# Kernel optimization log

Measured on AMD Instinct MI355X. Metric: run time of the kernel, lower is better.

Reference implementation:

```python
import jax, jax.numpy as jnp
import numpy as np

N = 50000          # nodes
E = 1_600_000      # edges (avg degree 32)
D = 128            # in_channels
H = 4              # heads
C = 32             # out_channels per head (H*C == D for residual add)
NEG_SLOPE = 0.2
STEPS = 3


def setup_inputs() -> dict:
    key = jax.random.key(0)
    k1, k2, k3, k4, k5 = jax.random.split(key, 5)
    x = jax.random.normal(k1, (N, D), jnp.float32)
    edge_index = jax.random.randint(k2, (2, E), 0, N)  # row0=src, row1=dst
    W = jax.random.normal(k3, (D, H * C), jnp.float32) * (1.0 / np.sqrt(D))
    a_src = jax.random.normal(k4, (H, C), jnp.float32) * 0.1
    a_dst = jax.random.normal(k5, (H, C), jnp.float32) * 0.1
    return {"x": x, "edge_index": edge_index, "W": W,
            "a_src": a_src, "a_dst": a_dst, "steps": STEPS}


def _attn_conv(x, edge_index, W, a_src, a_dst):
    """One GAT-style attention conv. Returns (out [N,H*C], attn [E,H], logits [E,H])."""
    src, dst = edge_index[0], edge_index[1]
    h = (x @ W).reshape(N, H, C)                      # [N,H,C]
    alpha_src = jnp.einsum('nhc,hc->nh', h, a_src)    # [N,H]
    alpha_dst = jnp.einsum('nhc,hc->nh', h, a_dst)    # [N,H]
    logits = jax.nn.leaky_relu(alpha_src[src] + alpha_dst[dst], NEG_SLOPE)  # [E,H]
    # softmax over incoming edges of each destination node (segment softmax)
    m = jax.ops.segment_max(logits, dst, num_segments=N)      # [N,H]
    m = jnp.where(jnp.isfinite(m), m, 0.0)                    # nodes w/o in-edges
    e = jnp.exp(logits - m[dst])                              # [E,H]
    denom = jax.ops.segment_sum(e, dst, num_segments=N)       # [N,H]
    attn = e / (denom[dst] + 1e-16)                           # [E,H]
    msg = h[src] * attn[..., None]                            # [E,H,C]
    out = jax.ops.segment_sum(msg, dst, num_segments=N)       # [N,H,C]
    return out.reshape(N, H * C), attn, logits


def reference(x, edge_index, W, a_src, a_dst, steps):
    x_s, attn_s, rel_s = [], [], []
    for _ in range(steps):  # fixed small step count, matches the torch Python loop
        x_prime, attn_t, rel_t = _attn_conv(x, edge_index, W, a_src, a_dst)
        x = x + x_prime
        x_s.append(x)
        attn_s.append(attn_t)
        rel_s.append(rel_t)
    return jnp.stack(x_s, 0), jnp.stack(attn_s, 0), jnp.stack(rel_s, 0)
```

## Files before the change

### kernel.cpp

```cpp
#include <hip/hip_runtime.h>
#include <hip/hip_bf16.h>
#include <math.h>

#define NN 50000
#define EE 1600000
#define DD 128
#define HH 4
#define NSTEP 3
#define NEG 0.2f
#define BM 32
#define NPB 8
#define CAPN 96
#define MAXD 96

typedef unsigned short ushort8v __attribute__((ext_vector_type(8)));
typedef float float4v __attribute__((ext_vector_type(4)));

__device__ __forceinline__ float leaky(float v) { return v >= 0.0f ? v : NEG * v; }

__device__ __forceinline__ unsigned short bfu(float f) {
    __hip_bfloat16 b = __float2bfloat16(f);
    return *reinterpret_cast<unsigned short*>(&b);
}
__device__ __forceinline__ float ubf(unsigned short u) {
    return __uint_as_float(((unsigned int)u) << 16);
}

__global__ __launch_bounds__(256) void gemm_k2(const float* __restrict__ X,
                                               const float* __restrict__ W,
                                               const float* __restrict__ a_src,
                                               const float* __restrict__ a_dst,
                                               unsigned short* __restrict__ Hb,
                                               float* __restrict__ as_,
                                               float4* __restrict__ nd) {
    __shared__ float xs[BM][132];
    const int tid  = threadIdx.x;
    const int tcol = tid & 31;
    const int trow = tid >> 5;
    const int row0 = blockIdx.x * BM;

    #pragma unroll
    for (int i = 0; i < 4; ++i) {
        const int l  = tid + 256 * i;
        const int r  = l >> 5;
        const int c4 = l & 31;
        float4 v = {0.f, 0.f, 0.f, 0.f};
        if (row0 + r < NN) v = ((const float4*)(X + (size_t)(row0 + r) * DD))[c4];
        *(float4*)&xs[r][c4 * 4] = v;
    }
    __syncthreads();

    const float4* __restrict__ W4 = (const float4*)W;
    float4 acc0 = {0,0,0,0}, acc1 = {0,0,0,0}, acc2 = {0,0,0,0}, acc3 = {0,0,0,0};

    for (int k = 0; k < DD; k += 4) {
        float4 wv0 = W4[(k + 0) * 32 + tcol];
        float4 wv1 = W4[(k + 1) * 32 + tcol];
        float4 wv2 = W4[(k + 2) * 32 + tcol];
        float4 wv3 = W4[(k + 3) * 32 + tcol];
        float4 xv0 = *(const float4*)&xs[4 * trow + 0][k];
        float4 xv1 = *(const float4*)&xs[4 * trow + 1][k];
        float4 xv2 = *(const float4*)&xs[4 * trow + 2][k];
        float4 xv3 = *(const float4*)&xs[4 * trow + 3][k];
        #define GSTEP(ACC, XV) \
            ACC.x += XV.x * wv0.x; ACC.y += XV.x * wv0.y; ACC.z += XV.x * wv0.z; ACC.w += XV.x * wv0.w; \
            ACC.x += XV.y * wv1.x; ACC.y += XV.y * wv1.y; ACC.z += XV.y * wv1.z; ACC.w += XV.y * wv1.w; \
            ACC.x += XV.z * wv2.x; ACC.y += XV.z * wv2.y; ACC.z += XV.z * wv2.z; ACC.w += XV.z * wv2.w; \
            ACC.x += XV.w * wv3.x; ACC.y += XV.w * wv3.y; ACC.z += XV.w * wv3.z; ACC.w += XV.w * wv3.w;
        GSTEP(acc0, xv0) GSTEP(acc1, xv1) GSTEP(acc2, xv2) GSTEP(acc3, xv3)
        #undef GSTEP
    }

    const float4 asv = ((const float4*)a_src)[tcol];
    const float4 adv = ((const float4*)a_dst)[tcol];
    float ps0 = acc0.x*asv.x + acc0.y*asv.y + acc0.z*asv.z + acc0.w*asv.w;
    float ps1 = acc1.x*asv.x + acc1.y*asv.y + acc1.z*asv.z + acc1.w*asv.w;
    float ps2 = acc2.x*asv.x + acc2.y*asv.y + acc2.z*asv.z + acc2.w*asv.w;
    float ps3 = acc3.x*asv.x + acc3.y*asv.y + acc3.z*asv.z + acc3.w*asv.w;
    float pd0 = acc0.x*adv.x + acc0.y*adv.y + acc0.z*adv.z + acc0.w*adv.w;
    float pd1 = acc1.x*adv.x + acc1.y*adv.y + acc1.z*adv.z + acc1.w*adv.w;
    float pd2 = acc2.x*adv.x + acc2.y*adv.y + acc2.z*adv.z + acc2.w*adv.w;
    float pd3 = acc3.x*adv.x + acc3.y*adv.y + acc3.z*adv.z + acc3.w*adv.w;
    #pragma unroll
    for (int off = 1; off < 8; off <<= 1) {
        ps0 += __shfl_xor(ps0, off); ps1 += __shfl_xor(ps1, off);
        ps2 += __shfl_xor(ps2, off); ps3 += __shfl_xor(ps3, off);
        pd0 += __shfl_xor(pd0, off); pd1 += __shfl_xor(pd1, off);
        pd2 += __shfl_xor(pd2, off); pd3 += __shfl_xor(pd3, off);
    }

    #pragma unroll
    for (int i = 0; i < 4; ++i) {
        const int row = row0 + 4 * trow + i;
        if (row >= NN) break;
        const float4 a = (i == 0) ? acc0 : (i == 1) ? acc1 : (i == 2) ? acc2 : acc3;
        ushort4 p;
        p.x = bfu(a.x); p.y = bfu(a.y); p.z = bfu(a.z); p.w = bfu(a.w);
        *(ushort4*)&Hb[(size_t)row * DD + 4 * tcol] = p;
    }
    if ((tcol & 7) == 0) {
        const int head = tcol >> 3;
        #pragma unroll
        for (int i = 0; i < 4; ++i) {
            const int row = row0 + 4 * trow + i;
            if (row >= NN) break;
            const float ps = (i == 0) ? ps0 : (i == 1) ? ps1 : (i == 2) ? ps2 : ps3;
            const float pd = (i == 0) ? pd0 : (i == 1) ? pd1 : (i == 2) ? pd2 : pd3;
            as_[(size_t)row * HH + head] = ps;
            ((float*)(nd + (size_t)row * 3))[head] = pd;
        }
    }
}

__global__ __launch_bounds__(256) void zero_k(int* __restrict__ p, int n) {
    const int i = blockIdx.x * 256 + threadIdx.x;
    if (i < n) p[i] = 0;
}

__global__ __launch_bounds__(256) void scat_k(const int* __restrict__ ei,
                                              int* __restrict__ cursor,
                                              int* __restrict__ csr) {
    const int e = blockIdx.x * 256 + threadIdx.x;
    if (e >= EE) return;
    const int s = ei[e], d = ei[EE + e];
    const int pos = atomicAdd(&cursor[d], 1);
    if (pos < MAXD) csr[(size_t)d * MAXD + pos] = s;
}

__global__ __launch_bounds__(256) void node_k3(const int* __restrict__ cursor,
                                               const int* __restrict__ csr,
                                               const float* __restrict__ as_,
                                               float4* __restrict__ nd,
                                               const unsigned short* __restrict__ Hb,
                                               const float* __restrict__ xprev,
                                               float* __restrict__ xout) {
    __shared__ int    src_l[NPB][CAPN];
    __shared__ float4 exp_l[NPB][CAPN];

    const int tid  = threadIdx.x;
    const int nl   = tid >> 5;
    const int lane = tid & 31;
    const int n    = blockIdx.x * NPB + nl;

    int deg = cursor[n];
    if (deg > MAXD) deg = MAXD;
    const size_t row0 = (size_t)n * MAXD;

    if (deg == 0) {
        ((float4*)(xout + (size_t)n * DD))[lane] = ((const float4*)(xprev + (size_t)n * DD))[lane];
        return;
    }

    const float4 adv = nd[(size_t)n * 3];

    float4 mx = {-INFINITY, -INFINITY, -INFINITY, -INFINITY};
    for (int j = lane; j < deg; j += 32) {
        const int s = csr[row0 + j];
        const float4 av = *(const float4*)(as_ + (size_t)s * HH);
        float4 l;
        l.x = leaky(av.x + adv.x); l.y = leaky(av.y + adv.y);
        l.z = leaky(av.z + adv.z); l.w = leaky(av.w + adv.w);
        src_l[nl][j] = s; exp_l[nl][j] = l;
        mx.x = fmaxf(mx.x, l.x); mx.y = fmaxf(mx.y, l.y);
        mx.z = fmaxf(mx.z, l.z); mx.w = fmaxf(mx.w, l.w);
    }
    #pragma unroll
    for (int off = 1; off < 32; off <<= 1) {
        mx.x = fmaxf(mx.x, __shfl_xor(mx.x, off));
        mx.y = fmaxf(mx.y, __shfl_xor(mx.y, off));
        mx.z = fmaxf(mx.z, __shfl_xor(mx.z, off));
        mx.w = fmaxf(mx.w, __shfl_xor(mx.w, off));
    }

    float4 ds = {0.f, 0.f, 0.f, 0.f};
    for (int j = lane; j < deg; j += 32) {
        const float4 l = exp_l[nl][j];
        float4 e4;
        e4.x = expf(l.x - mx.x); e4.y = expf(l.y - mx.y);
        e4.z = expf(l.z - mx.z); e4.w = expf(l.w - mx.w);
        exp_l[nl][j] = e4;
        ds.x += e4.x; ds.y += e4.y; ds.z += e4.z; ds.w += e4.w;
    }
    #pragma unroll
    for (int off = 1; off < 32; off <<= 1) {
        ds.x += __shfl_xor(ds.x, off); ds.y += __shfl_xor(ds.y, off);
        ds.z += __shfl_xor(ds.z, off); ds.w += __shfl_xor(ds.w, off);
    }
    float4 inv;
    inv.x = 1.0f / (ds.x + 1e-16f); inv.y = 1.0f / (ds.y + 1e-16f);
    inv.z = 1.0f / (ds.z + 1e-16f); inv.w = 1.0f / (ds.w + 1e-16f);

    if (lane == 0) {
        nd[(size_t)n * 3 + 1] = mx;
        nd[(size_t)n * 3 + 2] = inv;
    }

    const int esel = lane >> 4;
    const int sub  = lane & 15;
    const int hsel = sub >> 2;
    const float invh = (hsel == 0) ? inv.x : (hsel == 1) ? inv.y : (hsel == 2) ? inv.z : inv.w;
    float4 aclo = {0.f, 0.f, 0.f, 0.f};
    float4 achi = {0.f, 0.f, 0.f, 0.f};
    int j0 = 0;
    #pragma unroll 2
    for (; j0 + 2 <= deg; j0 += 2) {
        const int j = j0 + esel;
        const int s = src_l[nl][j];
        const float a = ((const float*)&exp_l[nl][j])[hsel] * invh;
        const ushort8v hv = *(const ushort8v*)&Hb[(size_t)s * DD + 8 * sub];
        aclo.x += ubf(hv[0]) * a; aclo.y += ubf(hv[1]) * a;
        aclo.z += ubf(hv[2]) * a; aclo.w += ubf(hv[3]) * a;
        achi.x += ubf(hv[4]) * a; achi.y += ubf(hv[5]) * a;
        achi.z += ubf(hv[6]) * a; achi.w += ubf(hv[7]) * a;
    }
    if (j0 < deg && esel == 0) {
        const int j = j0;
        const int s = src_l[nl][j];
        const float a = ((const float*)&exp_l[nl][j])[hsel] * invh;
        const ushort8v hv = *(const ushort8v*)&Hb[(size_t)s * DD + 8 * sub];
        aclo.x += ubf(hv[0]) * a; aclo.y += ubf(hv[1]) * a;
        aclo.z += ubf(hv[2]) * a; aclo.w += ubf(hv[3]) * a;
        achi.x += ubf(hv[4]) * a; achi.y += ubf(hv[5]) * a;
        achi.z += ubf(hv[6]) * a; achi.w += ubf(hv[7]) * a;
    }
    aclo.x += __shfl_xor(aclo.x, 16); aclo.y += __shfl_xor(aclo.y, 16);
    aclo.z += __shfl_xor(aclo.z, 16); aclo.w += __shfl_xor(aclo.w, 16);
    achi.x += __shfl_xor(achi.x, 16); achi.y += __shfl_xor(achi.y, 16);
    achi.z += __shfl_xor(achi.z, 16); achi.w += __shfl_xor(achi.w, 16);
    const float4 mine = (esel == 0) ? aclo : achi;
    const int fidx = 2 * sub + esel;
    const float4 xv = ((const float4*)(xprev + (size_t)n * DD))[fidx];
    float4 o;
    o.x = xv.x + mine.x; o.y = xv.y + mine.y; o.z = xv.z + mine.z; o.w = xv.w + mine.w;
    ((float4*)(xout + (size_t)n * DD))[fidx] = o;
}

__global__ __launch_bounds__(256) void edgeattn3_k(const int* __restrict__ ei,
                                                   const float* __restrict__ as3,
                                                   const float4* __restrict__ nd3,
                                                   float* __restrict__ rel_out,
                                                   float* __restrict__ attn_out) {
    const int e = blockIdx.x * 256 + threadIdx.x;
    if (e >= EE) return;
    const int st = blockIdx.y;
    const int s = __builtin_nontemporal_load(ei + e);
    const int d = __builtin_nontemporal_load(ei + EE + e);
    const float4 av = *(const float4*)(as3 + ((size_t)st * NN + s) * HH);
    const float4* ndp = nd3 + ((size_t)st * NN + d) * 3;
    const float4 dv = ndp[0];
    const float4 mm = ndp[1];
    const float4 iv = ndp[2];
    float4v l;
    l.x = leaky(av.x + dv.x); l.y = leaky(av.y + dv.y);
    l.z = leaky(av.z + dv.z); l.w = leaky(av.w + dv.w);
    __builtin_nontemporal_store(l, (float4v*)(rel_out + ((size_t)st * EE + e) * HH));
    float4v a;
    a.x = expf(l.x - mm.x) * iv.x; a.y = expf(l.y - mm.y) * iv.y;
    a.z = expf(l.z - mm.z) * iv.z; a.w = expf(l.w - mm.w) * iv.w;
    __builtin_nontemporal_store(a, (float4v*)(attn_out + ((size_t)st * EE + e) * HH));
}

extern "C" void kernel_launch(void* const* d_in, const int* in_sizes, int n_in,
                              void* d_out, int out_size, void* d_ws, size_t ws_size,
                              hipStream_t stream) {
    const float* x     = (const float*)d_in[0];
    const int*   ei    = (const int*)d_in[1];
    const float* W     = (const float*)d_in[2];
    const float* a_src = (const float*)d_in[3];
    const float* a_dst = (const float*)d_in[4];

    float* xs_out   = (float*)d_out;
    float* attn_out = xs_out + (size_t)NSTEP * NN * DD;
    float* rel_out  = attn_out + (size_t)NSTEP * EE * HH;

    unsigned short* hb = (unsigned short*)d_ws;
    float*  as3   = (float*)(hb + (size_t)NN * DD);
    float4* nd3   = (float4*)(as3 + (size_t)NSTEP * NN * HH);
    int*    cursor = (int*)(nd3 + (size_t)NSTEP * NN * 3);
    int*    csr    = cursor + NN;

    zero_k<<<(NN + 255) / 256, 256, 0, stream>>>(cursor, NN);
    scat_k<<<(EE + 255) / 256, 256, 0, stream>>>(ei, cursor, csr);

    const float* xprev = x;
    for (int s = 0; s < NSTEP; ++s) {
        float* xs_s = xs_out + (size_t)s * NN * DD;
        float* as_  = as3 + (size_t)s * NN * HH;
        float4* nd  = nd3 + (size_t)s * NN * 3;

        gemm_k2<<<(NN + BM - 1) / BM, 256, 0, stream>>>(xprev, W, a_src, a_dst, hb, as_, nd);
        node_k3<<<NN / NPB, 256, 0, stream>>>(cursor, csr, as_, nd, hb, xprev, xs_s);
        xprev = xs_s;
    }
    dim3 eg((EE + 255) / 256, NSTEP);
    edgeattn3_k<<<eg, 256, 0, stream>>>(ei, as3, nd3, rel_out, attn_out);
}
```

Measured before the change: 502.3 us.

## Split per-node CSR into edge-hashed partitions with 16-bit source indices

```diff
diff --git a/kernel.cpp b/kernel.cpp
--- a/kernel.cpp
+++ b/kernel.cpp
@@ -10,8 +10,9 @@
 #define NEG 0.2f
 #define BM 32
 #define NPB 8
-#define CAPN 96
-#define MAXD 96
+#define CAPN 128
+#define NPART 4
+#define SEGC 32
 
 typedef unsigned short ushort8v __attribute__((ext_vector_type(8)));
 typedef float float4v __attribute__((ext_vector_type(4)));
@@ -119,16 +120,17 @@
 
 __global__ __launch_bounds__(256) void scat_k(const int* __restrict__ ei,
                                               int* __restrict__ cursor,
-                                              int* __restrict__ csr) {
+                                              unsigned short* __restrict__ csr) {
     const int e = blockIdx.x * 256 + threadIdx.x;
     if (e >= EE) return;
     const int s = ei[e], d = ei[EE + e];
-    const int pos = atomicAdd(&cursor[d], 1);
-    if (pos < MAXD) csr[(size_t)d * MAXD + pos] = s;
+    const int c = d * NPART + (e & (NPART - 1));
+    const int pos = atomicAdd(&cursor[c], 1);
+    if (pos < SEGC) csr[(size_t)c * SEGC + pos] = (unsigned short)s;
 }
 
 __global__ __launch_bounds__(256) void node_k3(const int* __restrict__ cursor,
-                                               const int* __restrict__ csr,
+                                               const unsigned short* __restrict__ csr,
                                                const float* __restrict__ as_,
                                                float4* __restrict__ nd,
                                                const unsigned short* __restrict__ Hb,
@@ -142,9 +144,16 @@
     const int lane = tid & 31;
     const int n    = blockIdx.x * NPB + nl;
 
-    int deg = cursor[n];
-    if (deg > MAXD) deg = MAXD;
-    const size_t row0 = (size_t)n * MAXD;
+    const int cbase = n * NPART;
+    int degs[NPART];
+    int deg = 0;
+    #pragma unroll
+    for (int p = 0; p < NPART; ++p) {
+        int dp = cursor[cbase + p];
+        if (dp > SEGC) dp = SEGC;
+        degs[p] = dp;
+        deg += dp;
+    }
 
     if (deg == 0) {
         ((float4*)(xout + (size_t)n * DD))[lane] = ((const float4*)(xprev + (size_t)n * DD))[lane];
@@ -154,22 +163,27 @@
     const float4 adv = nd[(size_t)n * 3];
 
     float4 mx = {-INFINITY, -INFINITY, -INFINITY, -INFINITY};
-    for (int j = lane; j < deg; j += 32) {
-        const int s = csr[row0 + j];
-        const float4 av = *(const float4*)(as_ + (size_t)s * HH);
-        float4 l;
-        l.x = leaky(av.x + adv.x); l.y = leaky(av.y + adv.y);
-        l.z = leaky(av.z + adv.z); l.w = leaky(av.w + adv.w);
-        src_l[nl][j] = s; exp_l[nl][j] = l;
-        mx.x = fmaxf(mx.x, l.x); mx.y = fmaxf(mx.y, l.y);
-        mx.z = fmaxf(mx.z, l.z); mx.w = fmaxf(mx.w, l.w);
-    }
-    #pragma unroll
-    for (int off = 1; off < 32; off <<= 1) {
-        mx.x = fmaxf(mx.x, __shfl_xor(mx.x, off));
-        mx.y = fmaxf(mx.y, __shfl_xor(mx.y, off));
-        mx.z = fmaxf(mx.z, __shfl_xor(mx.z, off));
-        mx.w = fmaxf(mx.w, __shfl_xor(mx.w, off));
+    int off = 0;
+    #pragma unroll
+    for (int p = 0; p < NPART; ++p) {
+        if (lane < degs[p]) {
+            const int s = (int)csr[(size_t)(cbase + p) * SEGC + lane];
+            const float4 av = *(const float4*)(as_ + (size_t)s * HH);
+            float4 l;
+            l.x = leaky(av.x + adv.x); l.y = leaky(av.y + adv.y);
+            l.z = leaky(av.z + adv.z); l.w = leaky(av.w + adv.w);
+            src_l[nl][off + lane] = s; exp_l[nl][off + lane] = l;
+            mx.x = fmaxf(mx.x, l.x); mx.y = fmaxf(mx.y, l.y);
+            mx.z = fmaxf(mx.z, l.z); mx.w = fmaxf(mx.w, l.w);
+        }
+        off += degs[p];
+    }
+    #pragma unroll
+    for (int o = 1; o < 32; o <<= 1) {
+        mx.x = fmaxf(mx.x, __shfl_xor(mx.x, o));
+        mx.y = fmaxf(mx.y, __shfl_xor(mx.y, o));
+        mx.z = fmaxf(mx.z, __shfl_xor(mx.z, o));
+        mx.w = fmaxf(mx.w, __shfl_xor(mx.w, o));
     }
 
     float4 ds = {0.f, 0.f, 0.f, 0.f};
@@ -182,9 +196,9 @@
         ds.x += e4.x; ds.y += e4.y; ds.z += e4.z; ds.w += e4.w;
     }
     #pragma unroll
-    for (int off = 1; off < 32; off <<= 1) {
-        ds.x += __shfl_xor(ds.x, off); ds.y += __shfl_xor(ds.y, off);
-        ds.z += __shfl_xor(ds.z, off); ds.w += __shfl_xor(ds.w, off);
+    for (int o = 1; o < 32; o <<= 1) {
+        ds.x += __shfl_xor(ds.x, o); ds.y += __shfl_xor(ds.y, o);
+        ds.z += __shfl_xor(ds.z, o); ds.w += __shfl_xor(ds.w, o);
     }
     float4 inv;
     inv.x = 1.0f / (ds.x + 1e-16f); inv.y = 1.0f / (ds.y + 1e-16f);
@@ -277,9 +291,9 @@
     float*  as3   = (float*)(hb + (size_t)NN * DD);
     float4* nd3   = (float4*)(as3 + (size_t)NSTEP * NN * HH);
     int*    cursor = (int*)(nd3 + (size_t)NSTEP * NN * 3);
-    int*    csr    = cursor + NN;
-
-    zero_k<<<(NN + 255) / 256, 256, 0, stream>>>(cursor, NN);
+    unsigned short* csr = (unsigned short*)(cursor + (size_t)NN * NPART);
+
+    zero_k<<<(NN * NPART + 255) / 256, 256, 0, stream>>>(cursor, NN * NPART);
     scat_k<<<(EE + 255) / 256, 256, 0, stream>>>(ei, cursor, csr);
 
     const float* xprev = x;
```

Result: no change. 507.0 us (+0.9%).
